# Kernel tuning notes

Hardware: AMD Instinct MI355X
Metric: run time of the kernel (lower is better)

The kernel has to match this reference:

```python
import jax, jax.numpy as jnp
import numpy as np

B, E, N = 8, 256, 32          # triples, padded edges per triple, neighbors per edge
D, RD = 512, 768              # graph_dim, relation-semantic dim
R = 2000                      # num relations
L = 2                         # relation-context layers
K = 8                         # top_k neighbor similarity
M, HEADS = 32, 8              # memory tokens, memory-attention heads
HLLM = 4096                   # llm hidden size
EPS = 1e-5


def _ln(x, g, b):
    mu = jnp.mean(x, -1, keepdims=True)
    var = jnp.mean(jnp.square(x - mu), -1, keepdims=True)
    return (x - mu) * jax.lax.rsqrt(var + EPS) * g + b


def setup_inputs() -> dict:
    key = jax.random.key(0)
    ks = iter(jax.random.split(key, 40))
    nrm = lambda shape, s=0.02: jax.random.normal(next(ks), shape, jnp.float32) * s
    return {
        'edge_rel_ids': jax.random.randint(next(ks), (B, E), 0, R, jnp.int32),
        'neighbor_rel_ids': jax.random.randint(next(ks), (B, E, N), 0, R, jnp.int32),
        'edge_mask': jnp.ones((B, E), jnp.float32),
        'rel_emb': nrm((R, RD), 1.0),
        'rp_w': nrm((D, RD)), 'rp_b': jnp.zeros((D,), jnp.float32),
        'ly_vw': nrm((L, D, D)), 'ly_vb': jnp.zeros((L, D), jnp.float32),
        'ly_ow': nrm((L, D, D)), 'ly_ob': jnp.zeros((L, D), jnp.float32),
        'ly_n1g': jnp.ones((L, D), jnp.float32), 'ly_n1b': jnp.zeros((L, D), jnp.float32),
        'ly_n2g': jnp.ones((L, D), jnp.float32), 'ly_n2b': jnp.zeros((L, D), jnp.float32),
        'ly_w1': nrm((L, 4 * D, D)), 'ly_b1': jnp.zeros((L, 4 * D), jnp.float32),
        'ly_w2': nrm((L, D, 4 * D)), 'ly_b2': jnp.zeros((L, D), jnp.float32),
        'mem_q': nrm((M, D)),
        't_qw': nrm((D, D)), 't_qb': jnp.zeros((D,), jnp.float32),
        't_kw': nrm((D, D)), 't_kb': jnp.zeros((D,), jnp.float32),
        't_vw': nrm((D, D)), 't_vb': jnp.zeros((D,), jnp.float32),
        't_ow': nrm((D, D)), 't_ob': jnp.zeros((D,), jnp.float32),
        'proj_w': nrm((HLLM, D)), 'proj_b': jnp.zeros((HLLM,), jnp.float32),
    }


def reference(edge_rel_ids, neighbor_rel_ids, edge_mask, rel_emb, rp_w, rp_b,
              ly_vw, ly_vb, ly_ow, ly_ob, ly_n1g, ly_n1b, ly_n2g, ly_n2b,
              ly_w1, ly_b1, ly_w2, ly_b2, mem_q,
              t_qw, t_qb, t_kw, t_kb, t_vw, t_vb, t_ow, t_ob, proj_w, proj_b):
    rel_vector = lambda ids: rel_emb[ids] @ rp_w.T + rp_b  # embedding gather + rel_proj
    rel_vec = rel_vector(edge_rel_ids)            # [B,E,D]
    neigh = rel_vector(neighbor_rel_ids)          # [B,E,N,D] dominant gather traffic
    # per-edge cosine similarity to neighbor relations, top-k mean aggregation
    rn = rel_vec / jnp.maximum(jnp.linalg.norm(rel_vec, axis=-1, keepdims=True), 1e-12)
    nn_ = neigh / jnp.maximum(jnp.linalg.norm(neigh, axis=-1, keepdims=True), 1e-12)
    sims = jnp.einsum('bend,bed->ben', nn_, rn)   # [B,E,N]
    _, top_idx = jax.lax.top_k(sims, K)           # [B,E,K]
    agg = jnp.take_along_axis(neigh, top_idx[..., None], axis=2).mean(axis=2)  # [B,E,D]
    # RelationContextLayer stack. Each layer attends from one edge-state token to a
    # single context token: softmax over one key is identically 1, so the MHA
    # reduces exactly to out_proj(v_proj(context)) -- same math as torch MHA here.
    states = rel_vec
    for l in range(L):
        attn = (agg @ ly_vw[l].T + ly_vb[l]) @ ly_ow[l].T + ly_ob[l]
        states = _ln(states + attn, ly_n1g[l], ly_n1b[l])
        ff = jax.nn.gelu(states @ ly_w1[l].T + ly_b1[l], approximate=False) @ ly_w2[l].T + ly_b2[l]
        states = _ln(states + ff, ly_n2g[l], ly_n2b[l])
        states = states * edge_mask[..., None]
    # GraphMemoryTokenizer: learned queries cross-attend over padded edge states
    dh = D // HEADS
    q = (mem_q @ t_qw.T + t_qb).reshape(M, HEADS, dh)
    k = (states @ t_kw.T + t_kb).reshape(B, E, HEADS, dh)
    v = (states @ t_vw.T + t_vb).reshape(B, E, HEADS, dh)
    scores = jnp.einsum('mhd,behd->bhme', q, k) / jnp.sqrt(jnp.asarray(dh, q.dtype))
    scores = jnp.where(edge_mask[:, None, None, :] == 0, jnp.finfo(scores.dtype).min, scores)
    attnw = jax.nn.softmax(scores, axis=-1)
    mem = jnp.einsum('bhme,behd->bmhd', attnw, v).reshape(B, M, D)
    mem = mem @ t_ow.T + t_ob
    no_edges = jnp.sum(edge_mask, axis=1) == 0    # rows with zero edges -> zero memory
    mem = jnp.where(no_edges[:, None, None], 0.0, mem)
    return mem @ proj_w.T + proj_b                # [B,M,HLLM]
```

## Files before the change

### kernel.cpp

```cpp
#include <hip/hip_runtime.h>
#include <hip/hip_bf16.h>
#include <math.h>

#define B_   8
#define E_   256
#define N_   32
#define D_   512
#define RD_  768
#define R_   2000
#define L_   2
#define K_   8
#define M_   32
#define H_   8
#define DH_  64
#define HL_  4096

typedef float f32x4 __attribute__((ext_vector_type(4)));
typedef __bf16 bf16x8 __attribute__((ext_vector_type(8)));
typedef const __attribute__((address_space(1))) void GVoid;
typedef __attribute__((address_space(3))) void LVoid;

__device__ __forceinline__ float gelu_exact(float x) {
    return 0.5f * x * (1.0f + erff(x * 0.70710678118654752f));
}
__device__ __forceinline__ unsigned short f2bf(float x) {
    return __hip_bfloat16_raw(__float2bfloat16(x)).x;
}

template <int TM, int TN, int ACT_GELU, int OUT_BF16, int HAS_BIAS, int FLAGS, int SPLITK = 1>
__global__ __launch_bounds__(256) void gemm_mfma(const unsigned short* __restrict__ A,
                                                 const unsigned short* __restrict__ W,
                                                 const float* __restrict__ bias,
                                                 void* __restrict__ Cv,
                                                 int M, int N, int K,
                                                 const float* __restrict__ rowflag) {
    constexpr int WTM = TM / 2, WTN = TN / 2;
    constexpr int RM = WTM / 16, RN = WTN / 16;
    constexpr int AI = TM / 32, BI = TN / 32;
    __shared__ __align__(16) unsigned short As[2 * TM * 64];
    __shared__ __align__(16) unsigned short Bs[2 * TN * 64];

    const int tid = threadIdx.x;
    const int wave = tid >> 6, lane = tid & 63;
    const int quad = lane >> 4, l16 = lane & 15;
    const int wm = wave >> 1, wn = wave & 1;
    const int bm = blockIdx.y * TM, bn = blockIdx.x * TN;
    const int bz = (SPLITK > 1) ? blockIdx.z : 0;
    const int sub = lane >> 3;
    const int cpr = (lane & 7) ^ sub;

    f32x4 acc[RM][RN];
#pragma unroll
    for (int i = 0; i < RM; i++)
#pragma unroll
        for (int j = 0; j < RN; j++) acc[i][j] = (f32x4){0.f, 0.f, 0.f, 0.f};

    const int kspan = K / SPLITK;
    const int kb = bz * kspan;
    const int nt = kspan / 64;

    auto stage = [&](int k0, int buf) {
#pragma unroll
        for (int i = 0; i < AI; i++) {
            int r0 = (wave * AI + i) * 8;
            const unsigned short* g = A + (size_t)(bm + r0 + sub) * K + k0 + cpr * 8;
            __builtin_amdgcn_global_load_lds((GVoid*)g, (LVoid*)&As[buf * TM * 64 + r0 * 64], 16, 0, 0);
        }
#pragma unroll
        for (int i = 0; i < BI; i++) {
            int r0 = (wave * BI + i) * 8;
            const unsigned short* g = W + (size_t)(bn + r0 + sub) * K + k0 + cpr * 8;
            __builtin_amdgcn_global_load_lds((GVoid*)g, (LVoid*)&Bs[buf * TN * 64 + r0 * 64], 16, 0, 0);
        }
    };

    stage(kb, 0);
    __syncthreads();

    for (int t = 0; t < nt; t++) {
        const int cur = t & 1;
// ... 14 lines not shown
                bf[j] = *(const bf16x8*)&Bs[cur * TN * 64 + r * 64 + ch * 8];
            }
#pragma unroll
            for (int i = 0; i < RM; i++)
#pragma unroll
                for (int j = 0; j < RN; j++)
                    acc[i][j] = __builtin_amdgcn_mfma_f32_16x16x32_bf16(af[i], bf[j], acc[i][j], 0, 0, 0);
        }
        __syncthreads();
    }

    float* Cf = (float*)Cv + (size_t)bz * M * N;
#pragma unroll
    for (int i = 0; i < RM; i++) {
#pragma unroll
        for (int j = 0; j < RN; j++) {
            int c = bn + wn * WTN + j * 16 + l16;
            float bv = (HAS_BIAS && bz == 0) ? bias[c] : 0.f;
#pragma unroll
            for (int reg = 0; reg < 4; reg++) {
                int r = bm + wm * WTM + i * 16 + quad * 4 + reg;
                if (r < M) {
                    float v = acc[i][j][reg] + bv;
                    if (ACT_GELU) v = gelu_exact(v);
                    if (FLAGS) v *= rowflag[r >> 5];
                    if (OUT_BF16)
                        ((unsigned short*)Cv)[(size_t)r * N + c] = f2bf(v);
                    else
                        Cf[(size_t)r * N + c] = v;
                }
            }
        }
    }
}

__global__ __launch_bounds__(256) void projwfuse_kernel(
        const unsigned short* __restrict__ rel_bf, const unsigned short* __restrict__ rpw_bf,
        const float* __restrict__ rp_b, float* __restrict__ proj,
        const unsigned short* __restrict__ ow_bf, const unsigned short* __restrict__ vwT_bf,
        unsigned short* __restrict__ wfuse) {
    __shared__ __align__(16) unsigned short As[2 * 32 * 64];
    __shared__ __align__(16) unsigned short Bs[2 * 64 * 64];

    const unsigned short *A, *W;
    const float* bias;
    int Mg, Kg, bm, bn, obf;
    void* C;
    int t = blockIdx.x;
    if (t < 504) {
        A = rel_bf; W = rpw_bf; bias = rp_b; Mg = R_; Kg = RD_;
        C = proj; obf = 0; bn = (t & 7) * 64; bm = (t >> 3) * 32;
    } else {
        int u = t - 504, z = u >> 7, uu = u & 127;
        A = ow_bf + (size_t)z * 262144; W = vwT_bf + (size_t)z * 262144;
        bias = nullptr; Mg = 512; Kg = 512;
        C = wfuse + (size_t)z * 262144; obf = 1; bn = (uu & 7) * 64; bm = (uu >> 3) * 32;
    }

    const int tid = threadIdx.x;
    const int wave = tid >> 6, lane = tid & 63;
    const int quad = lane >> 4, l16 = lane & 15;
    const int wm = wave >> 1, wn = wave & 1;
    const int sub = lane >> 3;
    const int cpr = (lane & 7) ^ sub;

    f32x4 acc[2];
// ... 123 lines not shown
        for (int n = tid; n < 512; n += 256) {
            a.kvb[n] = a.t_kb[n];
            a.kvb[n + 512] = a.t_vb[n];
        }
        for (int b = 0; b < B_; b++) {
            float s = a.edge_mask[b * E_ + tid];
#pragma unroll
            for (int off = 32; off; off >>= 1) s += __shfl_xor(s, off, 64);
            if ((tid & 63) == 0) red[tid >> 6] = s;
            __syncthreads();
            if (tid == 0)
                a.flags[b] = (red[0] + red[1] + red[2] + red[3] == 0.f) ? 0.f : 1.f;
            __syncthreads();
        }
        return;
    }
    bx -= 1;
    {
        int wid = bx * 4 + (tid >> 6);
        int m = wid >> 9, n = wid & 511, lane = tid & 63;
        const float* ar = a.mem_q + (size_t)m * 512;
        const float* br = a.t_qw + (size_t)n * 512;
        float s = 0.f;
#pragma unroll
        for (int j = 0; j < 8; j++) s += ar[lane + 64 * j] * br[lane + 64 * j];
#pragma unroll
        for (int off = 32; off; off >>= 1) s += __shfl_xor(s, off, 64);
        if (lane == 0) a.qbuf[(size_t)m * 512 + n] = s + a.t_qb[n];
    }
}

__global__ void sim_topk_agg(const int* __restrict__ eids, const int* __restrict__ nids,
                             const float* __restrict__ proj,
                             unsigned short* __restrict__ agg_bf, float* __restrict__ states) {
    int be = blockIdx.x, tid = threadIdx.x;
    __shared__ float ev[512];
    __shared__ float sims[32];
    __shared__ int nid_s[32];
    __shared__ int sel[8];

    int eid = eids[be];
    const float* ep = proj + (size_t)eid * D_;
    float e0 = ep[tid], e1 = ep[tid + 256];
    ev[tid] = e0; ev[tid + 256] = e1;
    states[(size_t)be * D_ + tid] = e0;
    states[(size_t)be * D_ + tid + 256] = e1;
    if (tid < 32) nid_s[tid] = nids[be * N_ + tid];
    __syncthreads();

    int wid = tid >> 6, lane = tid & 63;
    float se = 0.f;
#pragma unroll
    for (int j = 0; j < 8; j++) { float v = ev[lane + 64 * j]; se += v * v; }
#pragma unroll
    for (int off = 32; off; off >>= 1) se += __shfl_xor(se, off, 64);
    float en = fmaxf(sqrtf(se), 1e-12f);

    for (int n = wid; n < N_; n += 4) {
        int nid = nid_s[n];
        const float* np = proj + (size_t)nid * D_;
        float s = 0.f, s2 = 0.f;
#pragma unroll
        for (int j = 0; j < 8; j++) {
            float v = np[lane + 64 * j];
            s += v * ev[lane + 64 * j];
            s2 += v * v;
        }
#pragma unroll
        for (int off = 32; off; off >>= 1) {
            s += __shfl_xor(s, off, 64);
            s2 += __shfl_xor(s2, off, 64);
        }
        if (lane == 0) sims[n] = s / (fmaxf(sqrtf(s2), 1e-12f) * en);
    }
    __syncthreads();

    if (tid < 64) {
        float v = (tid < 32) ? sims[tid] : -3.402823466e38f;
        int idx = tid;
        for (int k = 0; k < K_; k++) {
            float bv = v; int bi = idx;
#pragma unroll
            for (int off = 32; off; off >>= 1) {
                float ov = __shfl_xor(bv, off, 64);
                int oi = __shfl_xor(bi, off, 64);
                if (ov > bv || (ov == bv && oi < bi)) { bv = ov; bi = oi; }
            }
            if (tid == 0) sel[k] = nid_s[bi];
            if (idx == bi) v = -3.402823466e38f;
        }
    }
    __syncthreads();

    float a0 = 0.f, a1 = 0.f;
#pragma unroll
    for (int k = 0; k < K_; k++) {
        const float* sp = proj + (size_t)sel[k] * D_;
        a0 += sp[tid]; a1 += sp[tid + 256];
    }
    agg_bf[(size_t)be * D_ + tid] = f2bf(a0 * 0.125f);
    agg_bf[(size_t)be * D_ + tid + 256] = f2bf(a1 * 0.125f);
}

__global__ void add_ln_kernel(const float* __restrict__ x, const float* __restrict__ y,
                              int ystride, const float* __restrict__ y2,
                              const float* __restrict__ g,
                              const float* __restrict__ bb, const float* __restrict__ mask,
                              float* __restrict__ out, unsigned short* __restrict__ out_bf) {
    int t = blockIdx.x, tid = threadIdx.x;
    const float* xr = x + (size_t)t * D_;
    const float* yr = y + (size_t)t * ystride;
    float x0 = xr[tid] + yr[tid];
    float x1 = xr[tid + 256] + yr[tid + 256];
    if (y2) {
        const float* y2r = y2 + (size_t)t * D_;
        x0 += y2r[tid];
        x1 += y2r[tid + 256];
    }
    __shared__ float red[8];
    float s = x0 + x1;
#pragma unroll
    for (int off = 32; off; off >>= 1) s += __shfl_xor(s, off, 64);
    int wid = tid >> 6;
    if ((tid & 63) == 0) red[wid] = s;
    __syncthreads();
    float mean = (red[0] + red[1] + red[2] + red[3]) * (1.f / 512.f);
    float d0 = x0 - mean, d1 = x1 - mean;
    float v = d0 * d0 + d1 * d1;
#pragma unroll
    for (int off = 32; off; off >>= 1) v += __shfl_xor(v, off, 64);
    if ((tid & 63) == 0) red[4 + wid] = v;
    __syncthreads();
    float var = (red[4] + red[5] + red[6] + red[7]) * (1.f / 512.f);
    float rs = rsqrtf(var + 1e-5f);
    float mv = mask ? mask[t] : 1.f;
    float o0 = (d0 * rs * g[tid] + bb[tid]) * mv;
    float o1 = (d1 * rs * g[tid + 256] + bb[tid + 256]) * mv;
    if (out) {
        out[(size_t)t * D_ + tid] = o0;
        out[(size_t)t * D_ + tid + 256] = o1;
    }
    out_bf[(size_t)t * D_ + tid] = f2bf(o0);
    out_bf[(size_t)t * D_ + tid + 256] = f2bf(o1);
}

__global__ void dbl_ln_kernel(const float* __restrict__ x, const float* __restrict__ y,
                              const float* __restrict__ y2,
                              const float* __restrict__ g2, const float* __restrict__ b2,
                              const float* __restrict__ mask,
                              const float* __restrict__ att, int astride,
                              const float* __restrict__ g1, const float* __restrict__ b1,
                              float* __restrict__ out, unsigned short* __restrict__ out_bf) {
    int t = blockIdx.x, tid = threadIdx.x;
    const float* xr = x + (size_t)t * D_;
    const float* yr = y + (size_t)t * D_;
    float x0 = xr[tid] + yr[tid];
    float x1 = xr[tid + 256] + yr[tid + 256];
    if (y2) {
        const float* y2r = y2 + (size_t)t * D_;
        x0 += y2r[tid];
        x1 += y2r[tid + 256];
    }
    __shared__ float red[8];
    int wid = tid >> 6;
    float s = x0 + x1;
#pragma unroll
    for (int off = 32; off; off >>= 1) s += __shfl_xor(s, off, 64);
    if ((tid & 63) == 0) red[wid] = s;
    __syncthreads();
    float mean = (red[0] + red[1] + red[2] + red[3]) * (1.f / 512.f);
    float d0 = x0 - mean, d1 = x1 - mean;
    float v = d0 * d0 + d1 * d1;
#pragma unroll
    for (int off = 32; off; off >>= 1) v += __shfl_xor(v, off, 64);
    if ((tid & 63) == 0) red[4 + wid] = v;
    __syncthreads();
    float var = (red[4] + red[5] + red[6] + red[7]) * (1.f / 512.f);
    float rs = rsqrtf(var + 1e-5f);
    float mv = mask[t];
    float t0 = (d0 * rs * g2[tid] + b2[tid]) * mv;
    float t1 = (d1 * rs * g2[tid + 256] + b2[tid + 256]) * mv;
    const float* ar = att + (size_t)t * astride;
    float y0 = t0 + ar[tid];
    float y1 = t1 + ar[tid + 256];
    __syncthreads();
    float s2 = y0 + y1;
#pragma unroll
    for (int off = 32; off; off >>= 1) s2 += __shfl_xor(s2, off, 64);
    if ((tid & 63) == 0) red[wid] = s2;
    __syncthreads();
    float mean2 = (red[0] + red[1] + red[2] + red[3]) * (1.f / 512.f);
    float e0 = y0 - mean2, e1 = y1 - mean2;
    float v2 = e0 * e0 + e1 * e1;
#pragma unroll
    for (int off = 32; off; off >>= 1) v2 += __shfl_xor(v2, off, 64);
    if ((tid & 63) == 0) red[4 + wid] = v2;
    __syncthreads();
    float var2 = (red[4] + red[5] + red[6] + red[7]) * (1.f / 512.f);
    float rs2 = rsqrtf(var2 + 1e-5f);
    float o0 = e0 * rs2 * g1[tid] + b1[tid];
    float o1 = e1 * rs2 * g1[tid + 256] + b1[tid + 256];
    out[(size_t)t * D_ + tid] = o0;
    out[(size_t)t * D_ + tid + 256] = o1;
    out_bf[(size_t)t * D_ + tid] = f2bf(o0);
    out_bf[(size_t)t * D_ + tid + 256] = f2bf(o1);
}

__global__ void mem_attn(const float* __restrict__ qb, const float* __restrict__ kv,
                         const float* __restrict__ mask, unsigned short* __restrict__ memb) {
    int idx = blockIdx.x;
    int b = idx & 7;
    int h = (idx >> 3) & 7;
    int mg = idx >> 6;
    int tid = threadIdx.x;
    __shared__ float qh[4][64];
    __shared__ float sc[4][256];
    __shared__ float redm[4][4];
    __shared__ float reds[4][4];
    __shared__ float oacc[4][4][64];

    {
        int i = tid >> 6, d = tid & 63;
        qh[i][d] = qb[(size_t)(mg * 4 + i) * D_ + h * DH_ + d];
    }
    float mk = mask[b * E_ + tid];
    __syncthreads();

    const float* kr = kv + ((size_t)(b * E_ + tid)) * 1024 + h * DH_;
    float s0 = 0.f, s1 = 0.f, s2 = 0.f, s3 = 0.f;
#pragma unroll
    for (int d = 0; d < DH_; d += 4) {
        float4 k4 = *(const float4*)(kr + d);
        s0 += k4.x * qh[0][d] + k4.y * qh[0][d + 1] + k4.z * qh[0][d + 2] + k4.w * qh[0][d + 3];
        s1 += k4.x * qh[1][d] + k4.y * qh[1][d + 1] + k4.z * qh[1][d + 2] + k4.w * qh[1][d + 3];
        s2 += k4.x * qh[2][d] + k4.y * qh[2][d + 1] + k4.z * qh[2][d + 2] + k4.w * qh[2][d + 3];
        s3 += k4.x * qh[3][d] + k4.y * qh[3][d + 1] + k4.z * qh[3][d + 2] + k4.w * qh[3][d + 3];
    }
    s0 *= 0.125f; s1 *= 0.125f; s2 *= 0.125f; s3 *= 0.125f;
    if (mk == 0.f) { s0 = s1 = s2 = s3 = -3.402823466e38f; }

    int wid = tid >> 6;
    float m0 = s0, m1 = s1, m2 = s2, m3 = s3;
#pragma unroll
    for (int off = 32; off; off >>= 1) {
        m0 = fmaxf(m0, __shfl_xor(m0, off, 64));
        m1 = fmaxf(m1, __shfl_xor(m1, off, 64));
        m2 = fmaxf(m2, __shfl_xor(m2, off, 64));
        m3 = fmaxf(m3, __shfl_xor(m3, off, 64));
    }
    if ((tid & 63) == 0) { redm[wid][0] = m0; redm[wid][1] = m1; redm[wid][2] = m2; redm[wid][3] = m3; }
    __syncthreads();
    m0 = fmaxf(fmaxf(redm[0][0], redm[1][0]), fmaxf(redm[2][0], redm[3][0]));
    m1 = fmaxf(fmaxf(redm[0][1], redm[1][1]), fmaxf(redm[2][1], redm[3][1]));
    m2 = fmaxf(fmaxf(redm[0][2], redm[1][2]), fmaxf(redm[2][2], redm[3][2]));
    m3 = fmaxf(fmaxf(redm[0][3], redm[1][3]), fmaxf(redm[2][3], redm[3][3]));
    float p0 = expf(s0 - m0), p1 = expf(s1 - m1), p2 = expf(s2 - m2), p3 = expf(s3 - m3);
    float u0 = p0, u1 = p1, u2 = p2, u3 = p3;
#pragma unroll
    for (int off = 32; off; off >>= 1) {
        u0 += __shfl_xor(u0, off, 64);
        u1 += __shfl_xor(u1, off, 64);
        u2 += __shfl_xor(u2, off, 64);
        u3 += __shfl_xor(u3, off, 64);
    }
    if ((tid & 63) == 0) { reds[wid][0] = u0; reds[wid][1] = u1; reds[wid][2] = u2; reds[wid][3] = u3; }
    __syncthreads();
    u0 = reds[0][0] + reds[1][0] + reds[2][0] + reds[3][0];
    u1 = reds[0][1] + reds[1][1] + reds[2][1] + reds[3][1];
    u2 = reds[0][2] + reds[1][2] + reds[2][2] + reds[3][2];
    u3 = reds[0][3] + reds[1][3] + reds[2][3] + reds[3][3];
    sc[0][tid] = p0 / u0;
    sc[1][tid] = p1 / u1;
    sc[2][tid] = p2 / u2;
    sc[3][tid] = p3 / u3;
    __syncthreads();

    int d = tid & 63, part = tid >> 6;
    const float* vcol = kv + ((size_t)(b * E_ + part * 64)) * 1024 + 512 + h * DH_ + d;
    float a0 = 0.f, a1 = 0.f, a2 = 0.f, a3 = 0.f;
#pragma unroll 8
    for (int e = 0; e < 64; e++) {
        float vv = vcol[(size_t)e * 1024];
        a0 += sc[0][part * 64 + e] * vv;
        a1 += sc[1][part * 64 + e] * vv;
        a2 += sc[2][part * 64 + e] * vv;
        a3 += sc[3][part * 64 + e] * vv;
    }
    oacc[part][0][d] = a0;
    oacc[part][1][d] = a1;
    oacc[part][2][d] = a2;
    oacc[part][3][d] = a3;
    __syncthreads();
    if (part == 0) {
#pragma unroll
        for (int i = 0; i < 4; i++)
            memb[((size_t)(b * M_ + mg * 4 + i)) * D_ + h * DH_ + d] =
                f2bf(oacc[0][i][d] + oacc[1][i][d] + oacc[2][i][d] + oacc[3][i][d]);
    }
}

extern "C" void kernel_launch(void* const* d_in, const int* in_sizes, int n_in,
                              void* d_out, int out_size, void* d_ws, size_t ws_size,
                              hipStream_t stream) {
    const int*   edge_rel_ids     = (const int*)d_in[0];
    const int*   neighbor_rel_ids = (const int*)d_in[1];
    const float* edge_mask        = (const float*)d_in[2];
    const float* rel_emb          = (const float*)d_in[3];
    const float* rp_w             = (const float*)d_in[4];
    const float* rp_b             = (const float*)d_in[5];
    const float* ly_vw            = (const float*)d_in[6];
    const float* ly_vb            = (const float*)d_in[7];
    const float* ly_ow            = (const float*)d_in[8];
    const float* ly_ob            = (const float*)d_in[9];
    const float* ly_n1g           = (const float*)d_in[10];
    const float* ly_n1b           = (const float*)d_in[11];
    const float* ly_n2g           = (const float*)d_in[12];
    const float* ly_n2b           = (const float*)d_in[13];
    const float* ly_w1            = (const float*)d_in[14];
    const float* ly_b1            = (const float*)d_in[15];
    const float* ly_w2            = (const float*)d_in[16];
    const float* ly_b2            = (const float*)d_in[17];
    const float* mem_q            = (const float*)d_in[18];
    const float* t_qw             = (const float*)d_in[19];
    const float* t_qb             = (const float*)d_in[20];
    const float* t_kw             = (const float*)d_in[21];
    const float* t_kb             = (const float*)d_in[22];
    const float* t_vw             = (const float*)d_in[23];
    const float* t_vb             = (const float*)d_in[24];
    const float* t_ow             = (const float*)d_in[25];
    const float* t_ob             = (const float*)d_in[26];
    const float* proj_w           = (const float*)d_in[27];
    const float* proj_b           = (const float*)d_in[28];
    float* out = (float*)d_out;
    (void)ws_size; (void)in_sizes; (void)n_in; (void)out_size;

    char* ws = (char*)d_ws;
    size_t off = 0;
    auto allocf = [&](size_t n) { float* p = (float*)(ws + off); off += ((n * 4 + 255) & ~(size_t)255); return p; };
    auto allocb = [&](size_t n) { unsigned short* p = (unsigned short*)(ws + off); off += ((n * 2 + 255) & ~(size_t)255); return p; };

    const int T = B_ * E_;

    float* states  = allocf((size_t)T * D_);
    float* statesX = allocf((size_t)T * D_);
    float* proj    = allocf((size_t)R_ * D_);
    float* tmpB    = allocf((size_t)T * D_ * 2);
    float* attnall = allocf((size_t)T * 2 * D_);
    float* qbuf    = allocf((size_t)M_ * D_);
    float* bfuse   = allocf(2 * D_);
    float* kvb     = allocf(2 * D_);
    float* flags   = allocf(B_);
    float* kvbuf   = attnall;

    unsigned short* rel_bf  = allocb((size_t)2048 * RD_);
    unsigned short* rpw_bf  = allocb((size_t)D_ * RD_);
    unsigned short* agg_bf  = allocb((size_t)T * D_);
    unsigned short* st_bf   = allocb((size_t)T * D_);
    unsigned short* ff1_bf  = allocb((size_t)T * 4 * D_);
    unsigned short* vwT_bf  = allocb((size_t)L_ * D_ * D_);
    unsigned short* ow_bf   = allocb((size_t)L_ * D_ * D_);
    unsigned short* wfuse   = allocb((size_t)L_ * D_ * D_);
    unsigned short* w1_bf   = allocb((size_t)L_ * 4 * D_ * D_);
    unsigned short* w2_bf   = allocb((size_t)L_ * 4 * D_ * D_);
    unsigned short* kvw_bf  = allocb((size_t)2 * D_ * D_);
    unsigned short* tow_bf  = allocb((size_t)D_ * D_);
    unsigned short* pw_bf   = allocb((size_t)HL_ * D_);
    unsigned short* memb_bf = allocb((size_t)B_ * M_ * D_);
    unsigned short* mem2_bf = allocb((size_t)B_ * M_ * D_);

    PrepArgs a;
    int sizes[9] = { R_ * RD_, D_ * RD_, L_ * D_ * D_, L_ * 4 * D_ * D_,
                     L_ * 4 * D_ * D_, D_ * D_, D_ * D_, D_ * D_, HL_ * D_ };
    const float* srcs[9] = { rel_emb, rp_w, ly_ow, ly_w1, ly_w2, t_kw, t_vw, t_ow, proj_w };
    unsigned short* dsts[9] = { rel_bf, rpw_bf, ow_bf, w1_bf, w2_bf,
                                kvw_bf, kvw_bf + (size_t)D_ * D_, tow_bf, pw_bf };
    int cum = 0;
    for (int i = 0; i < 9; i++) {
        a.src[i] = srcs[i]; a.dst[i] = dsts[i];
        a.cum4[i] = cum; cum += sizes[i] / 4;
    }
    a.cum4[9] = cum;
    a.total4 = cum;
    a.nb_cvt = (cum + 255) / 256;
    a.ly_vw = ly_vw; a.vwT = vwT_bf;
    a.ly_ow = ly_ow; a.ly_vb = ly_vb; a.ly_ob = ly_ob; a.bfuse = bfuse;
    a.t_kb = t_kb; a.t_vb = t_vb; a.kvb = kvb;
    a.edge_mask = edge_mask; a.flags = flags;
    a.mem_q = mem_q; a.t_qw = t_qw; a.t_qb = t_qb; a.qbuf = qbuf;
    int nblk = a.nb_cvt + 512 + 256 + 1 + 4096;
    prep_all<<<nblk, 256, 0, stream>>>(a);

    projwfuse_kernel<<<760, 256, 0, stream>>>(rel_bf, rpw_bf, rp_b, proj,
                                              ow_bf, vwT_bf, wfuse);

    sim_topk_agg<<<T, 256, 0, stream>>>(edge_rel_ids, neighbor_rel_ids, proj,
                                        agg_bf, states);

    gemm_mfma<64, 64, 0, 0, 1, 0><<<dim3(16, 32), 256, 0, stream>>>(
        agg_bf, wfuse, bfuse, attnall, T, 2 * D_, D_, nullptr);

    add_ln_kernel<<<T, 256, 0, stream>>>(states, attnall, 2 * D_, nullptr,
                                         ly_n1g, ly_n1b, nullptr, statesX, st_bf);
    gemm_mfma<64, 128, 1, 1, 1, 0><<<dim3(16, 32), 256, 0, stream>>>(
        st_bf, w1_bf, ly_b1, ff1_bf, T, 4 * D_, D_, nullptr);
    gemm_mfma<64, 64, 0, 0, 1, 0, 2><<<dim3(8, 32, 2), 256, 0, stream>>>(
        ff1_bf, w2_bf, ly_b2, tmpB, T, D_, 4 * D_, nullptr);
    dbl_ln_kernel<<<T, 256, 0, stream>>>(statesX, tmpB, tmpB + (size_t)T * D_,
                                         ly_n2g, ly_n2b, edge_mask,
                                         attnall + D_, 2 * D_, ly_n1g + D_, ly_n1b + D_,
                                         states, st_bf);
    gemm_mfma<64, 128, 1, 1, 1, 0><<<dim3(16, 32), 256, 0, stream>>>(
        st_bf, w1_bf + (size_t)4 * D_ * D_, ly_b1 + 4 * D_, ff1_bf, T, 4 * D_, D_, nullptr);
    gemm_mfma<64, 64, 0, 0, 1, 0, 2><<<dim3(8, 32, 2), 256, 0, stream>>>(
        ff1_bf, w2_bf + (size_t)4 * D_ * D_, ly_b2 + D_, tmpB, T, D_, 4 * D_, nullptr);
    add_ln_kernel<<<T, 256, 0, stream>>>(states, tmpB, D_, tmpB + (size_t)T * D_,
                                         ly_n2g + D_, ly_n2b + D_, edge_mask,
                                         nullptr, st_bf);
    gemm_mfma<64, 64, 0, 0, 1, 0><<<dim3(16, 32), 256, 0, stream>>>(
        st_bf, kvw_bf, kvb, kvbuf, T, 2 * D_, D_, nullptr);
    mem_attn<<<B_ * H_ * (M_ / 4), 256, 0, stream>>>(qbuf, kvbuf, edge_mask, memb_bf);
    gemm_mfma<32, 64, 0, 1, 1, 1><<<dim3(8, 8), 256, 0, stream>>>(
        memb_bf, tow_bf, t_ob, mem2_bf, B_ * M_, D_, D_, flags);
    gemm_mfma<32, 64, 0, 0, 1, 0><<<dim3(64, 8), 256, 0, stream>>>(
        mem2_bf, pw_bf, proj_b, out, B_ * M_, HL_, D_, nullptr);
}
```

Baseline: 293.5 us.

## Fuse post-aggregation pipeline into persistent megakernel with grid barriers

Replaces the chain of about a dozen GEMM, layernorm and attention launches with one persistent kernel of 512 blocks. Stages are separated by atomic global barriers. The layernorm stages are rewritten to handle one row per wave with vectorized loads, and the states copy in sim_topk_agg is dropped by reading proj directly. This removes per-launch overhead and launch gaps, but adds spin-barrier cost and relies on all 512 blocks being co-resident (two per CU).

```diff
diff --git a/kernel.cpp b/kernel.cpp
--- a/kernel.cpp
+++ b/kernel.cpp
@@ -15,6 +15,8 @@
 #define DH_  64
 #define HL_  4096
 
+#define NBLK 512
+
 typedef float f32x4 __attribute__((ext_vector_type(4)));
 typedef __bf16 bf16x8 __attribute__((ext_vector_type(8)));
 typedef const __attribute__((address_space(1))) void GVoid;
@@ -27,25 +29,35 @@
     return __hip_bfloat16_raw(__float2bfloat16(x)).x;
 }
 
-template <int TM, int TN, int ACT_GELU, int OUT_BF16, int HAS_BIAS, int FLAGS, int SPLITK = 1>
-__global__ __launch_bounds__(256) void gemm_mfma(const unsigned short* __restrict__ A,
-                                                 const unsigned short* __restrict__ W,
-                                                 const float* __restrict__ bias,
-                                                 void* __restrict__ Cv,
-                                                 int M, int N, int K,
-                                                 const float* __restrict__ rowflag) {
+__device__ __forceinline__ void gbar(int* bar) {
+    __syncthreads();
+    if (threadIdx.x == 0) {
+        __threadfence();
+        __hip_atomic_fetch_add(bar, 1, __ATOMIC_RELEASE, __HIP_MEMORY_SCOPE_AGENT);
+        while (__hip_atomic_load(bar, __ATOMIC_ACQUIRE, __HIP_MEMORY_SCOPE_AGENT) < NBLK)
+            __builtin_amdgcn_s_sleep(2);
+        __threadfence();
+    }
+    __syncthreads();
+}
+
+template <int TM, int TN, int ACT_GELU, int OUT_BF16, int HAS_BIAS, int FLAGS, int SPLITK>
+__device__ __forceinline__ void gemm_tile(int bx, int by, int bz,
+        const unsigned short* __restrict__ A, const unsigned short* __restrict__ W,
+        const float* __restrict__ bias, void* __restrict__ Cv,
+        int M, int N, int K, const float* __restrict__ rowflag,
+        unsigned short* smem) {
     constexpr int WTM = TM / 2, WTN = TN / 2;
     constexpr int RM = WTM / 16, RN = WTN / 16;
     constexpr int AI = TM / 32, BI = TN / 32;
-    __shared__ __align__(16) unsigned short As[2 * TM * 64];
-    __shared__ __align__(16) unsigned short Bs[2 * TN * 64];
+    unsigned short* As = smem;
+    unsigned short* Bs = smem + 2 * TM * 64;
 
     const int tid = threadIdx.x;
     const int wave = tid >> 6, lane = tid & 63;
     const int quad = lane >> 4, l16 = lane & 15;
     const int wm = wave >> 1, wn = wave & 1;
-    const int bm = blockIdx.y * TM, bn = blockIdx.x * TN;
-    const int bz = (SPLITK > 1) ? blockIdx.z : 0;
+    const int bm = by * TM, bn = bx * TN;
     const int sub = lane >> 3;
     const int cpr = (lane & 7) ^ sub;
 
@@ -126,6 +138,281 @@
             }
         }
     }
+}
+
+__device__ __forceinline__ void wave_ln(const float* __restrict__ xr,
+                                        const float* __restrict__ yr,
+                                        const float* __restrict__ y2r,
+                                        const float* __restrict__ g,
+                                        const float* __restrict__ bb, float mv,
+                                        float* __restrict__ outf,
+                                        unsigned short* __restrict__ outb, int lane) {
+    int base = lane * 8;
+    float v[8];
+    {
+        float4 xa = *(const float4*)(xr + base), xb = *(const float4*)(xr + base + 4);
+        float4 ya = *(const float4*)(yr + base), yb = *(const float4*)(yr + base + 4);
+        v[0] = xa.x + ya.x; v[1] = xa.y + ya.y; v[2] = xa.z + ya.z; v[3] = xa.w + ya.w;
+        v[4] = xb.x + yb.x; v[5] = xb.y + yb.y; v[6] = xb.z + yb.z; v[7] = xb.w + yb.w;
+    }
+    if (y2r) {
+        float4 za = *(const float4*)(y2r + base), zb = *(const float4*)(y2r + base + 4);
+        v[0] += za.x; v[1] += za.y; v[2] += za.z; v[3] += za.w;
+        v[4] += zb.x; v[5] += zb.y; v[6] += zb.z; v[7] += zb.w;
+    }
+    float s = ((v[0] + v[1]) + (v[2] + v[3])) + ((v[4] + v[5]) + (v[6] + v[7]));
+#pragma unroll
+    for (int off = 32; off; off >>= 1) s += __shfl_xor(s, off, 64);
+    float mean = s * (1.f / 512.f);
+    float d[8], q = 0.f;
+#pragma unroll
+    for (int j = 0; j < 8; j++) { d[j] = v[j] - mean; q += d[j] * d[j]; }
+#pragma unroll
+    for (int off = 32; off; off >>= 1) q += __shfl_xor(q, off, 64);
+    float rs = rsqrtf(q * (1.f / 512.f) + 1e-5f);
+    float4 ga = *(const float4*)(g + base), gb = *(const float4*)(g + base + 4);
+    float4 ba = *(const float4*)(bb + base), bb4 = *(const float4*)(bb + base + 4);
+    float o[8];
+    o[0] = (d[0] * rs * ga.x + ba.x) * mv;  o[1] = (d[1] * rs * ga.y + ba.y) * mv;
+    o[2] = (d[2] * rs * ga.z + ba.z) * mv;  o[3] = (d[3] * rs * ga.w + ba.w) * mv;
+    o[4] = (d[4] * rs * gb.x + bb4.x) * mv; o[5] = (d[5] * rs * gb.y + bb4.y) * mv;
+    o[6] = (d[6] * rs * gb.z + bb4.z) * mv; o[7] = (d[7] * rs * gb.w + bb4.w) * mv;
+    if (outf) {
+        *(float4*)(outf + base) = make_float4(o[0], o[1], o[2], o[3]);
+        *(float4*)(outf + base + 4) = make_float4(o[4], o[5], o[6], o[7]);
+    }
+    union { unsigned short u[8]; uint4 q4; } pk;
+#pragma unroll
+    for (int j = 0; j < 8; j++) pk.u[j] = f2bf(o[j]);
+    *(uint4*)(outb + base) = pk.q4;
+}
+
+__device__ __forceinline__ void mem_attn_tile(int idx, const float* __restrict__ qb,
+        const float* __restrict__ kv, const float* __restrict__ mask,
+        unsigned short* __restrict__ memb, unsigned short* smemraw) {
+    float* SM = (float*)smemraw;
+    float* qh = SM;
+    float* sc = SM + 256;
+    float* redm = SM + 1280;
+    float* reds = SM + 1296;
+    float* oacc = SM + 1312;
+    int b = idx & 7, h = (idx >> 3) & 7, mg = idx >> 6;
+    int tid = threadIdx.x;
+
+    { int i = tid >> 6, d = tid & 63; qh[i * 64 + d] = qb[(size_t)(mg * 4 + i) * D_ + h * DH_ + d]; }
+    float mk = mask[b * E_ + tid];
+    __syncthreads();
+
+    const float* kr = kv + ((size_t)(b * E_ + tid)) * 1024 + h * DH_;
+    float s0 = 0.f, s1 = 0.f, s2 = 0.f, s3 = 0.f;
+#pragma unroll
+    for (int d = 0; d < DH_; d += 4) {
+        float4 k4 = *(const float4*)(kr + d);
+        s0 += k4.x * qh[d] + k4.y * qh[d + 1] + k4.z * qh[d + 2] + k4.w * qh[d + 3];
+        s1 += k4.x * qh[64 + d] + k4.y * qh[64 + d + 1] + k4.z * qh[64 + d + 2] + k4.w * qh[64 + d + 3];
+        s2 += k4.x * qh[128 + d] + k4.y * qh[128 + d + 1] + k4.z * qh[128 + d + 2] + k4.w * qh[128 + d + 3];
+        s3 += k4.x * qh[192 + d] + k4.y * qh[192 + d + 1] + k4.z * qh[192 + d + 2] + k4.w * qh[192 + d + 3];
+    }
+    s0 *= 0.125f; s1 *= 0.125f; s2 *= 0.125f; s3 *= 0.125f;
+    if (mk == 0.f) { s0 = s1 = s2 = s3 = -3.402823466e38f; }
+
+    int wid = tid >> 6;
+    float m0 = s0, m1 = s1, m2 = s2, m3 = s3;
+#pragma unroll
+    for (int off = 32; off; off >>= 1) {
+        m0 = fmaxf(m0, __shfl_xor(m0, off, 64));
+        m1 = fmaxf(m1, __shfl_xor(m1, off, 64));
+        m2 = fmaxf(m2, __shfl_xor(m2, off, 64));
+        m3 = fmaxf(m3, __shfl_xor(m3, off, 64));
+    }
+    if ((tid & 63) == 0) { redm[wid * 4 + 0] = m0; redm[wid * 4 + 1] = m1; redm[wid * 4 + 2] = m2; redm[wid * 4 + 3] = m3; }
+    __syncthreads();
+    m0 = fmaxf(fmaxf(redm[0], redm[4]), fmaxf(redm[8], redm[12]));
+    m1 = fmaxf(fmaxf(redm[1], redm[5]), fmaxf(redm[9], redm[13]));
+    m2 = fmaxf(fmaxf(redm[2], redm[6]), fmaxf(redm[10], redm[14]));
+    m3 = fmaxf(fmaxf(redm[3], redm[7]), fmaxf(redm[11], redm[15]));
+    float p0 = expf(s0 - m0), p1 = expf(s1 - m1), p2 = expf(s2 - m2), p3 = expf(s3 - m3);
+    float u0 = p0, u1 = p1, u2 = p2, u3 = p3;
+#pragma unroll
+    for (int off = 32; off; off >>= 1) {
+        u0 += __shfl_xor(u0, off, 64);
+        u1 += __shfl_xor(u1, off, 64);
+        u2 += __shfl_xor(u2, off, 64);
+        u3 += __shfl_xor(u3, off, 64);
+    }
+    if ((tid & 63) == 0) { reds[wid * 4 + 0] = u0; reds[wid * 4 + 1] = u1; reds[wid * 4 + 2] = u2; reds[wid * 4 + 3] = u3; }
+    __syncthreads();
+    u0 = reds[0] + reds[4] + reds[8] + reds[12];
+    u1 = reds[1] + reds[5] + reds[9] + reds[13];
+    u2 = reds[2] + reds[6] + reds[10] + reds[14];
+    u3 = reds[3] + reds[7] + reds[11] + reds[15];
+    sc[0 * 256 + tid] = p0 / u0;
+    sc[1 * 256 + tid] = p1 / u1;
+    sc[2 * 256 + tid] = p2 / u2;
+    sc[3 * 256 + tid] = p3 / u3;
+    __syncthreads();
+
+    int d = tid & 63, part = tid >> 6;
+    const float* vcol = kv + ((size_t)(b * E_ + part * 64)) * 1024 + 512 + h * DH_ + d;
+    float a0 = 0.f, a1 = 0.f, a2 = 0.f, a3 = 0.f;
+#pragma unroll 8
+    for (int e = 0; e < 64; e++) {
+        float vv = vcol[(size_t)e * 1024];
+        a0 += sc[0 * 256 + part * 64 + e] * vv;
+        a1 += sc[1 * 256 + part * 64 + e] * vv;
+        a2 += sc[2 * 256 + part * 64 + e] * vv;
+        a3 += sc[3 * 256 + part * 64 + e] * vv;
+    }
+    oacc[(part * 4 + 0) * 64 + d] = a0;
+    oacc[(part * 4 + 1) * 64 + d] = a1;
+    oacc[(part * 4 + 2) * 64 + d] = a2;
+    oacc[(part * 4 + 3) * 64 + d] = a3;
+    __syncthreads();
+    if (part == 0) {
+#pragma unroll
+        for (int i = 0; i < 4; i++)
+            memb[((size_t)(b * M_ + mg * 4 + i)) * D_ + h * DH_ + d] =
+                f2bf(oacc[(0 * 4 + i) * 64 + d] + oacc[(1 * 4 + i) * 64 + d] +
+                     oacc[(2 * 4 + i) * 64 + d] + oacc[(3 * 4 + i) * 64 + d]);
+    }
+}
+
+struct MegaArgs {
+    const unsigned short *agg, *wfuse, *w1, *w2, *kvw, *tow, *pw;
+    const float *bfuse, *b1, *b2, *n1g, *n1b, *n2g, *n2b, *mask, *kvb, *qbuf,
+                *tob, *projb, *flags, *proj;
+    const int* eids;
+    float *attnall, *statesX, *states, *tmpB;
+    unsigned short *st, *ff1, *memb, *mem2;
+    float* out;
+    int* bar;
+};
+
+__global__ __launch_bounds__(256, 2) void mega_kernel(MegaArgs a) {
+    __shared__ __align__(16) unsigned short SMEM[24576];
+    const int tile = blockIdx.x;
+    const int tid = threadIdx.x;
+    const int wv = tid >> 6, lane = tid & 63;
+
+    gemm_tile<64, 64, 0, 0, 1, 0, 1>(tile & 15, tile >> 4, 0, a.agg, a.wfuse,
+                                     a.bfuse, a.attnall, 2048, 1024, 512, nullptr, SMEM);
+    gbar(a.bar + 0);
+
+    {
+        int t = (tile << 2) | wv;
+        const float* xr = a.proj + (size_t)a.eids[t] * D_;
+        const float* yr = a.attnall + (size_t)t * 1024;
+        wave_ln(xr, yr, nullptr, a.n1g, a.n1b, 1.f,
+                a.statesX + (size_t)t * D_, a.st + (size_t)t * D_, lane);
+    }
+    gbar(a.bar + 1);
+
+    gemm_tile<64, 128, 1, 1, 1, 0, 1>(tile & 15, tile >> 4, 0, a.st, a.w1, a.b1,
+                                      a.ff1, 2048, 2048, 512, nullptr, SMEM);
+    gbar(a.bar + 2);
+
+    { int r = tile & 255;
+      gemm_tile<64, 64, 0, 0, 1, 0, 2>(r & 7, r >> 3, tile >> 8, a.ff1, a.w2, a.b2,
+                                       a.tmpB, 2048, 512, 2048, nullptr, SMEM); }
+    gbar(a.bar + 3);
+
+    {
+        int t = (tile << 2) | wv;
+        int base = lane * 8;
+        const float* xr = a.statesX + (size_t)t * D_;
+        const float* yr = a.tmpB + (size_t)t * D_;
+        const float* zr = a.tmpB + (size_t)2048 * D_ + (size_t)t * D_;
+        float v[8];
+        {
+            float4 xa = *(const float4*)(xr + base), xb = *(const float4*)(xr + base + 4);
+            float4 ya = *(const float4*)(yr + base), yb = *(const float4*)(yr + base + 4);
+            float4 za = *(const float4*)(zr + base), zb = *(const float4*)(zr + base + 4);
+            v[0] = xa.x + ya.x + za.x; v[1] = xa.y + ya.y + za.y;
+            v[2] = xa.z + ya.z + za.z; v[3] = xa.w + ya.w + za.w;
+            v[4] = xb.x + yb.x + zb.x; v[5] = xb.y + yb.y + zb.y;
+            v[6] = xb.z + yb.z + zb.z; v[7] = xb.w + yb.w + zb.w;
+        }
+        float s = ((v[0] + v[1]) + (v[2] + v[3])) + ((v[4] + v[5]) + (v[6] + v[7]));
+#pragma unroll
+        for (int off = 32; off; off >>= 1) s += __shfl_xor(s, off, 64);
+        float mean = s * (1.f / 512.f);
+        float d[8], q = 0.f;
+#pragma unroll
+        for (int j = 0; j < 8; j++) { d[j] = v[j] - mean; q += d[j] * d[j]; }
+#pragma unroll
+        for (int off = 32; off; off >>= 1) q += __shfl_xor(q, off, 64);
+        float rs = rsqrtf(q * (1.f / 512.f) + 1e-5f);
+        float mv = a.mask[t];
+        float4 ga = *(const float4*)(a.n2g + base), gb = *(const float4*)(a.n2g + base + 4);
+        float4 ba = *(const float4*)(a.n2b + base), bb4 = *(const float4*)(a.n2b + base + 4);
+        const float* ar = a.attnall + (size_t)t * 1024 + 512;
+        float4 aa = *(const float4*)(ar + base), ab = *(const float4*)(ar + base + 4);
+        float w[8];
+        w[0] = (d[0] * rs * ga.x + ba.x) * mv + aa.x;  w[1] = (d[1] * rs * ga.y + ba.y) * mv + aa.y;
+        w[2] = (d[2] * rs * ga.z + ba.z) * mv + aa.z;  w[3] = (d[3] * rs * ga.w + ba.w) * mv + aa.w;
+        w[4] = (d[4] * rs * gb.x + bb4.x) * mv + ab.x; w[5] = (d[5] * rs * gb.y + bb4.y) * mv + ab.y;
+        w[6] = (d[6] * rs * gb.z + bb4.z) * mv + ab.z; w[7] = (d[7] * rs * gb.w + bb4.w) * mv + ab.w;
+        float s2 = ((w[0] + w[1]) + (w[2] + w[3])) + ((w[4] + w[5]) + (w[6] + w[7]));
+#pragma unroll
+        for (int off = 32; off; off >>= 1) s2 += __shfl_xor(s2, off, 64);
+        float mean2 = s2 * (1.f / 512.f);
+        float e[8], q2 = 0.f;
+#pragma unroll
+        for (int j = 0; j < 8; j++) { e[j] = w[j] - mean2; q2 += e[j] * e[j]; }
+#pragma unroll
+        for (int off = 32; off; off >>= 1) q2 += __shfl_xor(q2, off, 64);
+        float rs2 = rsqrtf(q2 * (1.f / 512.f) + 1e-5f);
+        float4 g1a = *(const float4*)(a.n1g + 512 + base), g1b = *(const float4*)(a.n1g + 512 + base + 4);
+        float4 b1a = *(const float4*)(a.n1b + 512 + base), b1b = *(const float4*)(a.n1b + 512 + base + 4);
+        float o[8];
+        o[0] = e[0] * rs2 * g1a.x + b1a.x; o[1] = e[1] * rs2 * g1a.y + b1a.y;
+        o[2] = e[2] * rs2 * g1a.z + b1a.z; o[3] = e[3] * rs2 * g1a.w + b1a.w;
+        o[4] = e[4] * rs2 * g1b.x + b1b.x; o[5] = e[5] * rs2 * g1b.y + b1b.y;
+        o[6] = e[6] * rs2 * g1b.z + b1b.z; o[7] = e[7] * rs2 * g1b.w + b1b.w;
+        float* outf = a.states + (size_t)t * D_;
+        *(float4*)(outf + base) = make_float4(o[0], o[1], o[2], o[3]);
+        *(float4*)(outf + base + 4) = make_float4(o[4], o[5], o[6], o[7]);
+        union { unsigned short u[8]; uint4 q4; } pk;
+#pragma unroll
+        for (int j = 0; j < 8; j++) pk.u[j] = f2bf(o[j]);
+        *(uint4*)(a.st + (size_t)t * D_ + base) = pk.q4;
+    }
+    gbar(a.bar + 4);
+
+    gemm_tile<64, 128, 1, 1, 1, 0, 1>(tile & 15, tile >> 4, 0, a.st,
+                                      a.w1 + (size_t)4 * D_ * D_, a.b1 + 4 * D_,
+                                      a.ff1, 2048, 2048, 512, nullptr, SMEM);
+    gbar(a.bar + 5);
+
+    { int r = tile & 255;
+      gemm_tile<64, 64, 0, 0, 1, 0, 2>(r & 7, r >> 3, tile >> 8, a.ff1,
+                                       a.w2 + (size_t)4 * D_ * D_, a.b2 + D_,
+                                       a.tmpB, 2048, 512, 2048, nullptr, SMEM); }
+    gbar(a.bar + 6);
+
+    {
+        int t = (tile << 2) | wv;
+        wave_ln(a.states + (size_t)t * D_, a.tmpB + (size_t)t * D_,
+                a.tmpB + (size_t)2048 * D_ + (size_t)t * D_,
+                a.n2g + D_, a.n2b + D_, a.mask[t],
+                nullptr, a.st + (size_t)t * D_, lane);
+    }
+    gbar(a.bar + 7);
+
+    gemm_tile<64, 64, 0, 0, 1, 0, 1>(tile & 15, tile >> 4, 0, a.st, a.kvw, a.kvb,
+                                     a.attnall, 2048, 1024, 512, nullptr, SMEM);
+    gbar(a.bar + 8);
+
+    mem_attn_tile(tile, a.qbuf, a.attnall, a.mask, a.memb, SMEM);
+    gbar(a.bar + 9);
+
+    if (tile < 64)
+        gemm_tile<32, 64, 0, 1, 1, 1, 1>(tile & 7, tile >> 3, 0, a.memb, a.tow,
+                                         a.tob, a.mem2, 256, 512, 512, a.flags, SMEM);
+    gbar(a.bar + 10);
+
+    gemm_tile<32, 64, 0, 0, 1, 0, 1>(tile & 63, tile >> 6, 0, a.mem2, a.pw,
+                                     a.projb, a.out, 256, 4096, 512, nullptr, SMEM);
 }
 
 __global__ __launch_bounds__(256) void projwfuse_kernel(
@@ -315,7 +602,7 @@
 
 __global__ void sim_topk_agg(const int* __restrict__ eids, const int* __restrict__ nids,
                              const float* __restrict__ proj,
-                             unsigned short* __restrict__ agg_bf, float* __restrict__ states) {
+                             unsigned short* __restrict__ agg_bf) {
     int be = blockIdx.x, tid = threadIdx.x;
     __shared__ float ev[512];
     __shared__ float sims[32];
@@ -324,10 +611,8 @@
 
     int eid = eids[be];
     const float* ep = proj + (size_t)eid * D_;
-    float e0 = ep[tid], e1 = ep[tid + 256];
-    ev[tid] = e0; ev[tid + 256] = e1;
-    states[(size_t)be * D_ + tid] = e0;
-    states[(size_t)be * D_ + tid + 256] = e1;
+    ev[tid] = ep[tid];
+    ev[tid + 256] = ep[tid + 256];
     if (tid < 32) nid_s[tid] = nids[be * N_ + tid];
     __syncthreads();
 
@@ -383,203 +668,6 @@
     }
     agg_bf[(size_t)be * D_ + tid] = f2bf(a0 * 0.125f);
     agg_bf[(size_t)be * D_ + tid + 256] = f2bf(a1 * 0.125f);
-}
-
-__global__ void add_ln_kernel(const float* __restrict__ x, const float* __restrict__ y,
-                              int ystride, const float* __restrict__ y2,
-                              const float* __restrict__ g,
-                              const float* __restrict__ bb, const float* __restrict__ mask,
-                              float* __restrict__ out, unsigned short* __restrict__ out_bf) {
-    int t = blockIdx.x, tid = threadIdx.x;
-    const float* xr = x + (size_t)t * D_;
-    const float* yr = y + (size_t)t * ystride;
-    float x0 = xr[tid] + yr[tid];
-    float x1 = xr[tid + 256] + yr[tid + 256];
-    if (y2) {
-        const float* y2r = y2 + (size_t)t * D_;
-        x0 += y2r[tid];
-        x1 += y2r[tid + 256];
-    }
-    __shared__ float red[8];
-    float s = x0 + x1;
-#pragma unroll
-    for (int off = 32; off; off >>= 1) s += __shfl_xor(s, off, 64);
-    int wid = tid >> 6;
-    if ((tid & 63) == 0) red[wid] = s;
-    __syncthreads();
-    float mean = (red[0] + red[1] + red[2] + red[3]) * (1.f / 512.f);
-    float d0 = x0 - mean, d1 = x1 - mean;
-    float v = d0 * d0 + d1 * d1;
-#pragma unroll
-    for (int off = 32; off; off >>= 1) v += __shfl_xor(v, off, 64);
-    if ((tid & 63) == 0) red[4 + wid] = v;
-    __syncthreads();
-    float var = (red[4] + red[5] + red[6] + red[7]) * (1.f / 512.f);
-    float rs = rsqrtf(var + 1e-5f);
-    float mv = mask ? mask[t] : 1.f;
-    float o0 = (d0 * rs * g[tid] + bb[tid]) * mv;
-    float o1 = (d1 * rs * g[tid + 256] + bb[tid + 256]) * mv;
-    if (out) {
-        out[(size_t)t * D_ + tid] = o0;
-        out[(size_t)t * D_ + tid + 256] = o1;
-    }
-    out_bf[(size_t)t * D_ + tid] = f2bf(o0);
-    out_bf[(size_t)t * D_ + tid + 256] = f2bf(o1);
-}
-
-__global__ void dbl_ln_kernel(const float* __restrict__ x, const float* __restrict__ y,
-                              const float* __restrict__ y2,
-                              const float* __restrict__ g2, const float* __restrict__ b2,
-                              const float* __restrict__ mask,
-                              const float* __restrict__ att, int astride,
-                              const float* __restrict__ g1, const float* __restrict__ b1,
-                              float* __restrict__ out, unsigned short* __restrict__ out_bf) {
-    int t = blockIdx.x, tid = threadIdx.x;
-    const float* xr = x + (size_t)t * D_;
-    const float* yr = y + (size_t)t * D_;
-    float x0 = xr[tid] + yr[tid];
-    float x1 = xr[tid + 256] + yr[tid + 256];
-    if (y2) {
-        const float* y2r = y2 + (size_t)t * D_;
-        x0 += y2r[tid];
-        x1 += y2r[tid + 256];
-    }
-    __shared__ float red[8];
-    int wid = tid >> 6;
-    float s = x0 + x1;
-#pragma unroll
-    for (int off = 32; off; off >>= 1) s += __shfl_xor(s, off, 64);
-    if ((tid & 63) == 0) red[wid] = s;
-    __syncthreads();
-    float mean = (red[0] + red[1] + red[2] + red[3]) * (1.f / 512.f);
-    float d0 = x0 - mean, d1 = x1 - mean;
-    float v = d0 * d0 + d1 * d1;
-#pragma unroll
-    for (int off = 32; off; off >>= 1) v += __shfl_xor(v, off, 64);
-    if ((tid & 63) == 0) red[4 + wid] = v;
-    __syncthreads();
-    float var = (red[4] + red[5] + red[6] + red[7]) * (1.f / 512.f);
-    float rs = rsqrtf(var + 1e-5f);
-    float mv = mask[t];
-    float t0 = (d0 * rs * g2[tid] + b2[tid]) * mv;
-    float t1 = (d1 * rs * g2[tid + 256] + b2[tid + 256]) * mv;
-    const float* ar = att + (size_t)t * astride;
-    float y0 = t0 + ar[tid];
-    float y1 = t1 + ar[tid + 256];
-    __syncthreads();
-    float s2 = y0 + y1;
-#pragma unroll
-    for (int off = 32; off; off >>= 1) s2 += __shfl_xor(s2, off, 64);
-    if ((tid & 63) == 0) red[wid] = s2;
-    __syncthreads();
-    float mean2 = (red[0] + red[1] + red[2] + red[3]) * (1.f / 512.f);
-    float e0 = y0 - mean2, e1 = y1 - mean2;
-    float v2 = e0 * e0 + e1 * e1;
-#pragma unroll
-    for (int off = 32; off; off >>= 1) v2 += __shfl_xor(v2, off, 64);
-    if ((tid & 63) == 0) red[4 + wid] = v2;
-    __syncthreads();
-    float var2 = (red[4] + red[5] + red[6] + red[7]) * (1.f / 512.f);
-    float rs2 = rsqrtf(var2 + 1e-5f);
-    float o0 = e0 * rs2 * g1[tid] + b1[tid];
-    float o1 = e1 * rs2 * g1[tid + 256] + b1[tid + 256];
-    out[(size_t)t * D_ + tid] = o0;
-    out[(size_t)t * D_ + tid + 256] = o1;
-    out_bf[(size_t)t * D_ + tid] = f2bf(o0);
-    out_bf[(size_t)t * D_ + tid + 256] = f2bf(o1);
-}
-
-__global__ void mem_attn(const float* __restrict__ qb, const float* __restrict__ kv,
-                         const float* __restrict__ mask, unsigned short* __restrict__ memb) {
-    int idx = blockIdx.x;
-    int b = idx & 7;
-    int h = (idx >> 3) & 7;
-    int mg = idx >> 6;
-    int tid = threadIdx.x;
-    __shared__ float qh[4][64];
-    __shared__ float sc[4][256];
-    __shared__ float redm[4][4];
-    __shared__ float reds[4][4];
-    __shared__ float oacc[4][4][64];
-
-    {
-        int i = tid >> 6, d = tid & 63;
-        qh[i][d] = qb[(size_t)(mg * 4 + i) * D_ + h * DH_ + d];
-    }
-    float mk = mask[b * E_ + tid];
-    __syncthreads();
-
-    const float* kr = kv + ((size_t)(b * E_ + tid)) * 1024 + h * DH_;
-    float s0 = 0.f, s1 = 0.f, s2 = 0.f, s3 = 0.f;
-#pragma unroll
-    for (int d = 0; d < DH_; d += 4) {
-        float4 k4 = *(const float4*)(kr + d);
-        s0 += k4.x * qh[0][d] + k4.y * qh[0][d + 1] + k4.z * qh[0][d + 2] + k4.w * qh[0][d + 3];
-        s1 += k4.x * qh[1][d] + k4.y * qh[1][d + 1] + k4.z * qh[1][d + 2] + k4.w * qh[1][d + 3];
-        s2 += k4.x * qh[2][d] + k4.y * qh[2][d + 1] + k4.z * qh[2][d + 2] + k4.w * qh[2][d + 3];
-        s3 += k4.x * qh[3][d] + k4.y * qh[3][d + 1] + k4.z * qh[3][d + 2] + k4.w * qh[3][d + 3];
-    }
-    s0 *= 0.125f; s1 *= 0.125f; s2 *= 0.125f; s3 *= 0.125f;
-    if (mk == 0.f) { s0 = s1 = s2 = s3 = -3.402823466e38f; }
-
-    int wid = tid >> 6;
-    float m0 = s0, m1 = s1, m2 = s2, m3 = s3;
-#pragma unroll
-    for (int off = 32; off; off >>= 1) {
-        m0 = fmaxf(m0, __shfl_xor(m0, off, 64));
-        m1 = fmaxf(m1, __shfl_xor(m1, off, 64));
-        m2 = fmaxf(m2, __shfl_xor(m2, off, 64));
-        m3 = fmaxf(m3, __shfl_xor(m3, off, 64));
-    }
-    if ((tid & 63) == 0) { redm[wid][0] = m0; redm[wid][1] = m1; redm[wid][2] = m2; redm[wid][3] = m3; }
-    __syncthreads();
-    m0 = fmaxf(fmaxf(redm[0][0], redm[1][0]), fmaxf(redm[2][0], redm[3][0]));
-    m1 = fmaxf(fmaxf(redm[0][1], redm[1][1]), fmaxf(redm[2][1], redm[3][1]));
-    m2 = fmaxf(fmaxf(redm[0][2], redm[1][2]), fmaxf(redm[2][2], redm[3][2]));
-    m3 = fmaxf(fmaxf(redm[0][3], redm[1][3]), fmaxf(redm[2][3], redm[3][3]));
-    float p0 = expf(s0 - m0), p1 = expf(s1 - m1), p2 = expf(s2 - m2), p3 = expf(s3 - m3);
-    float u0 = p0, u1 = p1, u2 = p2, u3 = p3;
-#pragma unroll
-    for (int off = 32; off; off >>= 1) {
-        u0 += __shfl_xor(u0, off, 64);
-        u1 += __shfl_xor(u1, off, 64);
-        u2 += __shfl_xor(u2, off, 64);
-        u3 += __shfl_xor(u3, off, 64);
-    }
-    if ((tid & 63) == 0) { reds[wid][0] = u0; reds[wid][1] = u1; reds[wid][2] = u2; reds[wid][3] = u3; }
-    __syncthreads();
-    u0 = reds[0][0] + reds[1][0] + reds[2][0] + reds[3][0];
-    u1 = reds[0][1] + reds[1][1] + reds[2][1] + reds[3][1];
-    u2 = reds[0][2] + reds[1][2] + reds[2][2] + reds[3][2];
-    u3 = reds[0][3] + reds[1][3] + reds[2][3] + reds[3][3];
-    sc[0][tid] = p0 / u0;
-    sc[1][tid] = p1 / u1;
-    sc[2][tid] = p2 / u2;
-    sc[3][tid] = p3 / u3;
-    __syncthreads();
-
-    int d = tid & 63, part = tid >> 6;
-    const float* vcol = kv + ((size_t)(b * E_ + part * 64)) * 1024 + 512 + h * DH_ + d;
-    float a0 = 0.f, a1 = 0.f, a2 = 0.f, a3 = 0.f;
-#pragma unroll 8
-    for (int e = 0; e < 64; e++) {
-        float vv = vcol[(size_t)e * 1024];
-        a0 += sc[0][part * 64 + e] * vv;
-        a1 += sc[1][part * 64 + e] * vv;
-        a2 += sc[2][part * 64 + e] * vv;
-        a3 += sc[3][part * 64 + e] * vv;
-    }
-    oacc[part][0][d] = a0;
-    oacc[part][1][d] = a1;
-    oacc[part][2][d] = a2;
-    oacc[part][3][d] = a3;
-    __syncthreads();
-    if (part == 0) {
-#pragma unroll
-        for (int i = 0; i < 4; i++)
-            memb[((size_t)(b * M_ + mg * 4 + i)) * D_ + h * DH_ + d] =
-                f2bf(oacc[0][i][d] + oacc[1][i][d] + oacc[2][i][d] + oacc[3][i][d]);
-    }
 }
 
 extern "C" void kernel_launch(void* const* d_in, const int* in_sizes, int n_in,
@@ -633,7 +721,7 @@
     float* bfuse   = allocf(2 * D_);
     float* kvb     = allocf(2 * D_);
     float* flags   = allocf(B_);
-    float* kvbuf   = attnall;
+    int*   barrier = (int*)allocf(64);
 
     unsigned short* rel_bf  = allocb((size_t)2048 * RD_);
     unsigned short* rpw_bf  = allocb((size_t)D_ * RD_);
@@ -651,6 +739,8 @@
     unsigned short* memb_bf = allocb((size_t)B_ * M_ * D_);
     unsigned short* mem2_bf = allocb((size_t)B_ * M_ * D_);
 
+    hipMemsetAsync(barrier, 0, 64 * sizeof(int), stream);
+
     PrepArgs a;
     int sizes[9] = { R_ * RD_, D_ * RD_, L_ * D_ * D_, L_ * 4 * D_ * D_,
                      L_ * 4 * D_ * D_, D_ * D_, D_ * D_, D_ * D_, HL_ * D_ };
@@ -676,34 +766,19 @@
     projwfuse_kernel<<<760, 256, 0, stream>>>(rel_bf, rpw_bf, rp_b, proj,
                                               ow_bf, vwT_bf, wfuse);
 
-    sim_topk_agg<<<T, 256, 0, stream>>>(edge_rel_ids, neighbor_rel_ids, proj,
-                                        agg_bf, states);
-
-    gemm_mfma<64, 64, 0, 0, 1, 0><<<dim3(16, 32), 256, 0, stream>>>(
-        agg_bf, wfuse, bfuse, attnall, T, 2 * D_, D_, nullptr);
-
-    add_ln_kernel<<<T, 256, 0, stream>>>(states, attnall, 2 * D_, nullptr,
-                                         ly_n1g, ly_n1b, nullptr, statesX, st_bf);
-    gemm_mfma<64, 128, 1, 1, 1, 0><<<dim3(16, 32), 256, 0, stream>>>(
-        st_bf, w1_bf, ly_b1, ff1_bf, T, 4 * D_, D_, nullptr);
-    gemm_mfma<64, 64, 0, 0, 1, 0, 2><<<dim3(8, 32, 2), 256, 0, stream>>>(
-        ff1_bf, w2_bf, ly_b2, tmpB, T, D_, 4 * D_, nullptr);
-    dbl_ln_kernel<<<T, 256, 0, stream>>>(statesX, tmpB, tmpB + (size_t)T * D_,
-                                         ly_n2g, ly_n2b, edge_mask,
-                                         attnall + D_, 2 * D_, ly_n1g + D_, ly_n1b + D_,
-                                         states, st_bf);
-    gemm_mfma<64, 128, 1, 1, 1, 0><<<dim3(16, 32), 256, 0, stream>>>(
-        st_bf, w1_bf + (size_t)4 * D_ * D_, ly_b1 + 4 * D_, ff1_bf, T, 4 * D_, D_, nullptr);
-    gemm_mfma<64, 64, 0, 0, 1, 0, 2><<<dim3(8, 32, 2), 256, 0, stream>>>(
-        ff1_bf, w2_bf + (size_t)4 * D_ * D_, ly_b2 + D_, tmpB, T, D_, 4 * D_, nullptr);
-    add_ln_kernel<<<T, 256, 0, stream>>>(states, tmpB, D_, tmpB + (size_t)T * D_,
-                                         ly_n2g + D_, ly_n2b + D_, edge_mask,
-                                         nullptr, st_bf);
-    gemm_mfma<64, 64, 0, 0, 1, 0><<<dim3(16, 32), 256, 0, stream>>>(
-        st_bf, kvw_bf, kvb, kvbuf, T, 2 * D_, D_, nullptr);
-    mem_attn<<<B_ * H_ * (M_ / 4), 256, 0, stream>>>(qbuf, kvbuf, edge_mask, memb_bf);
-    gemm_mfma<32, 64, 0, 1, 1, 1><<<dim3(8, 8), 256, 0, stream>>>(
-        memb_bf, tow_bf, t_ob, mem2_bf, B_ * M_, D_, D_, flags);
-    gemm_mfma<32, 64, 0, 0, 1, 0><<<dim3(64, 8), 256, 0, stream>>>(
-        mem2_bf, pw_bf, proj_b, out, B_ * M_, HL_, D_, nullptr);
-}
+    sim_topk_agg<<<T, 256, 0, stream>>>(edge_rel_ids, neighbor_rel_ids, proj, agg_bf);
+
+    MegaArgs m;
+    m.agg = agg_bf; m.wfuse = wfuse; m.w1 = w1_bf; m.w2 = w2_bf;
+    m.kvw = kvw_bf; m.tow = tow_bf; m.pw = pw_bf;
+    m.bfuse = bfuse; m.b1 = ly_b1; m.b2 = ly_b2;
+    m.n1g = ly_n1g; m.n1b = ly_n1b; m.n2g = ly_n2g; m.n2b = ly_n2b;
+    m.mask = edge_mask; m.kvb = kvb; m.qbuf = qbuf; m.tob = t_ob;
+    m.projb = proj_b; m.flags = flags; m.proj = proj;
+    m.eids = edge_rel_ids;
+    m.attnall = attnall; m.statesX = statesX; m.states = states; m.tmpB = tmpB;
+    m.st = st_bf; m.ff1 = ff1_bf; m.memb = memb_bf; m.mem2 = mem2_bf;
+    m.out = out;
+    m.bar = barrier;
+    mega_kernel<<<NBLK, 256, 0, stream>>>(m);
+}
```

Result: slower. 1.042 ms (+254.9%).
